# Kernel tuning notes

Hardware: AMD Instinct MI355X
Metric: run time of the kernel (lower is better)

## Reference

```python
import jax, jax.numpy as jnp
import numpy as np

EMBED_DIM = 512


def setup_inputs() -> dict:
    key = jax.random.key(0)
    k1, k2, k3 = jax.random.split(key, 3)
    B, T, E = 8, 2048, EMBED_DIM
    x = jax.random.normal(k1, (B, T, E), dtype=jnp.float32)
    # Linear weights stored [in, out] (torch stores [out, in]; math is identical via transpose)
    Wq = jax.random.normal(k2, (E, E), dtype=jnp.float32) * (E ** -0.5)
    bq = jnp.zeros((E,), dtype=jnp.float32)
    Wk = jax.random.normal(k3, (E, E), dtype=jnp.float32) * (E ** -0.5)
    bk = jnp.zeros((E,), dtype=jnp.float32)
    return {"x": x, "Wq": Wq, "bq": bq, "Wk": Wk, "bk": bk}


def reference(x, Wq, bq, Wk, bk) -> jnp.ndarray:
    scaling = jnp.float32(EMBED_DIM ** -0.5)
    q = (x @ Wq + bq) * scaling          # [B, T, E]
    k = x @ Wk + bk                       # [B, T, E]
    scores = jnp.einsum("bqe,bke->bqk", q, k)   # [B, T, T]
    attn = jax.nn.softmax(scores, axis=-1)
    return jnp.einsum("bqk,bke->bqe", attn, x)  # V = x
```

## Files before the change

kernel.cpp:

```cpp
#include <hip/hip_runtime.h>
#include <hip/hip_bf16.h>
#include <stdint.h>

#define B_  8
#define T_  2048
#define E_  512

typedef __attribute__((ext_vector_type(8))) __bf16 bf16x8;
typedef __attribute__((ext_vector_type(8))) unsigned short ushort8;
typedef __attribute__((ext_vector_type(4))) unsigned short ushort4v;
typedef __attribute__((ext_vector_type(4))) float f32x4;

__device__ __forceinline__ float bf2f(unsigned short u) {
  union { unsigned int u; float f; } c; c.u = ((unsigned int)u) << 16; return c.f;
}
__device__ __forceinline__ unsigned short f2bf(float f) {
  union { float f; unsigned int u; } c; c.f = f;
  unsigned int u = c.u;
  unsigned int r = (u + 0x7FFFu + ((u >> 16) & 1u)) >> 16;
  return (unsigned short)r;
}

__device__ __forceinline__ void gload_lds16(const void* g, void* l) {
  __builtin_amdgcn_global_load_lds(
      (const __attribute__((address_space(1))) uint32_t*)g,
      (__attribute__((address_space(3))) uint32_t*)l, 16, 0, 0);
}

__global__ __launch_bounds__(256)
void trans_conv_kernel(const float* __restrict__ x, unsigned short* __restrict__ xbf,
                       unsigned short* __restrict__ xT) {
  __shared__ unsigned short tile[64][66];
  const int t0 = blockIdx.x * 64, e0 = blockIdx.y * 64, b = blockIdx.z;
  const int tid = threadIdx.x;
  const float* xb = x + ((size_t)b * T_ + t0) * E_ + e0;
  unsigned short* xbf_b = xbf + ((size_t)b * T_ + t0) * E_ + e0;
#pragma unroll
  for (int it = 0; it < 4; ++it) {
    int tr = (tid >> 4) + it * 16;
    int ec = (tid & 15) * 4;
    float4 f = *reinterpret_cast<const float4*>(xb + (size_t)tr * E_ + ec);
    ushort4v o;
    o[0] = f2bf(f.x); o[1] = f2bf(f.y); o[2] = f2bf(f.z); o[3] = f2bf(f.w);
    *reinterpret_cast<ushort4v*>(xbf_b + (size_t)tr * E_ + ec) = o;
    tile[ec + 0][tr] = o[0];
    tile[ec + 1][tr] = o[1];
    tile[ec + 2][tr] = o[2];
    tile[ec + 3][tr] = o[3];
  }
  __syncthreads();
  unsigned short* dst = xT + ((size_t)b * E_ + e0) * T_ + t0;
#pragma unroll
  for (int it = 0; it < 2; ++it) {
    int er = (tid >> 3) + it * 32;
    int tg = (tid & 7) * 8;
    ushort8 r;
#pragma unroll
    for (int j = 0; j < 8; ++j) r[j] = tile[er][tg + j];
    *reinterpret_cast<ushort8*>(dst + (size_t)er * T_ + tg) = r;
  }
}

__global__ __launch_bounds__(256)
void conv_w_kernel(const float* __restrict__ Wq, const float* __restrict__ Wk,
                   const float* __restrict__ bq, const float* __restrict__ bk,
                   unsigned short* __restrict__ WT, float* __restrict__ bqk, float scale) {
  int idx = blockIdx.x * 256 + threadIdx.x;
  int n  = idx >> 9;
  int kk = idx & 511;
  float v = (n < E_) ? Wq[kk * E_ + n] * scale : Wk[kk * E_ + (n - E_)];
  WT[idx] = f2bf(v);
  if (idx < 2 * E_) {
    float bv = (idx < E_) ? bq[idx] * scale : bk[idx - E_];
    bqk[idx] = bv;
  }
}

#define STAGE_A(pbuf, kt) do {                                                  \
  _Pragma("unroll") for (int r_ = 0; r_ < 4; ++r_)                              \
    gload_lds16(gA + (long long)(r_ * 32) * lda + (long long)(kt) * 64,         \
                &sm[(pbuf) * 16384 + r_ * 2048 + tid * 8]);                     \
} while (0)

#define STAGE_B(pbuf, kt) do {                                                  \
  _Pragma("unroll") for (int r_ = 0; r_ < 4; ++r_)                              \
    gload_lds16(gB + (long long)(r_ * 32) * ldb + (long long)(kt) * 64,         \
                &sm[(pbuf) * 16384 + 8192 + r_ * 2048 + tid * 8]);              \
} while (0)

template<int OUT>
__global__ __launch_bounds__(256)
void gemm128c(const unsigned short* __restrict__ A, int lda, long long strA,
              const unsigned short* __restrict__ B, int ldb, long long strB,
              void* __restrict__ Cv, int ldc, long long strC,
              int K, const float* __restrict__ bias, int NBX, int NBY,
              float* __restrict__ Rg, const float* __restrict__ invR)
{
  __shared__ unsigned short sm[32768];
  const int tid  = threadIdx.x;
  const int lane = tid & 63;
  const int wv   = tid >> 6;
  const int wrp  = wv >> 1;
  const int wcp  = wv & 1;
  const int fr   = lane & 15;

  const int nwg = gridDim.x, bid = blockIdx.x;
  const int qq = nwg >> 3, rr = nwg & 7, xc = bid & 7, ii = bid >> 3;
  const int wg = (xc < rr ? xc * (qq + 1) : rr * (qq + 1) + (xc - rr) * qq) + ii;
  const int bx = wg % NBX;
  const int tt = wg / NBX;
  const int by = tt % NBY;
  const int bz = tt / NBY;

  const long long m0 = (long long)by * 128;
  const long long n0 = (long long)bx * 128;
  const unsigned short* Ab = A + (long long)bz * strA + m0 * lda;
  const unsigned short* Bb = B + (long long)bz * strB + n0 * ldb;

  const int srow = tid >> 3;
  const int scol = ((tid & 7) * 8) ^ ((srow & 7) << 3);
  const unsigned short* gA = Ab + (long long)srow * lda + scol;
  const unsigned short* gB = Bb + (long long)srow * ldb + scol;

  const int xorc  = (fr & 7) << 3;
  const int q8    = (lane >> 4) * 8;
  const int c0    = q8 ^ xorc;
  const int c1    = (32 + q8) ^ xorc;
  const int aRow  = (wrp * 64 + fr) * 64;
  const int bRow  = 8192 + (wcp * 64 + fr) * 64;

  f32x4 acc[4][4];
#pragma unroll
  for (int i = 0; i < 4; ++i)
#pragma unroll
    for (int j = 0; j < 4; ++j) acc[i][j] = (f32x4){0.f, 0.f, 0.f, 0.f};

  bf16x8 aA[4][2], bB2[2][2];
  const int NT = K >> 6;

  STAGE_A(0, 0);
  STAGE_B(0, 0);
  STAGE_A(1, 1);
  asm volatile("s_waitcnt vmcnt(4)" ::: "memory");
  __builtin_amdgcn_s_barrier();

  int p = 0;
  for (int t = 0; t < NT; ++t) {
    const int pb = p * 16384;
    const int pn = p ^ 1;
    if (t + 1 < NT) STAGE_B(pn, t + 1);
#pragma unroll
    for (int m = 0; m < 4; ++m) {
      aA[m][0] = *reinterpret_cast<const bf16x8*>(&sm[pb + aRow + m * 1024 + c0]);
      aA[m][1] = *reinterpret_cast<const bf16x8*>(&sm[pb + aRow + m * 1024 + c1]);
    }
#pragma unroll
    for (int n = 0; n < 2; ++n) {
      bB2[n][0] = *reinterpret_cast<const bf16x8*>(&sm[pb + bRow + n * 1024 + c0]);
      bB2[n][1] = *reinterpret_cast<const bf16x8*>(&sm[pb + bRow + n * 1024 + c1]);
    }
    __builtin_amdgcn_s_setprio(1);
#pragma unroll
    for (int m = 0; m < 4; ++m)
#pragma unroll
      for (int n = 0; n < 2; ++n) {
        acc[m][n] = __builtin_amdgcn_mfma_f32_16x16x32_bf16(aA[m][0], bB2[n][0], acc[m][n], 0, 0, 0);
        acc[m][n] = __builtin_amdgcn_mfma_f32_16x16x32_bf16(aA[m][1], bB2[n][1], acc[m][n], 0, 0, 0);
      }
    __builtin_amdgcn_s_setprio(0);
    __builtin_amdgcn_s_barrier();
    if (t + 2 < NT) STAGE_A(p, t + 2);
#pragma unroll
    for (int n = 0; n < 2; ++n) {
      bB2[n][0] = *reinterpret_cast<const bf16x8*>(&sm[pb + bRow + (2 + n) * 1024 + c0]);
      bB2[n][1] = *reinterpret_cast<const bf16x8*>(&sm[pb + bRow + (2 + n) * 1024 + c1]);
    }
    __builtin_amdgcn_s_setprio(1);
#pragma unroll
    for (int m = 0; m < 4; ++m)
#pragma unroll
      for (int n = 0; n < 2; ++n) {
        acc[m][2 + n] = __builtin_amdgcn_mfma_f32_16x16x32_bf16(aA[m][0], bB2[n][0], acc[m][2 + n], 0, 0, 0);
        acc[m][2 + n] = __builtin_amdgcn_mfma_f32_16x16x32_bf16(aA[m][1], bB2[n][1], acc[m][2 + n], 0, 0, 0);
      }
    __builtin_amdgcn_s_setprio(0);
    if (t + 2 < NT) asm volatile("s_waitcnt vmcnt(4)" ::: "memory");
    else            asm volatile("s_waitcnt vmcnt(0)" ::: "memory");
    __builtin_amdgcn_s_barrier();
    p = pn;
  }

  const int rq = (lane >> 4) * 4;
  if (OUT == 2) {
    float* Cb = (float*)Cv + (long long)bz * strC;
#pragma unroll
    for (int m = 0; m < 4; ++m)
#pragma unroll
      for (int j = 0; j < 4; ++j) {
        const int lrow = wrp * 64 + m * 16 + rq + j;
        const long long row = m0 + lrow;
        const float inv = invR[bz * 2048 + row];
#pragma unroll
        for (int n = 0; n < 4; ++n)
          Cb[row * ldc + n0 + wcp * 64 + n * 16 + fr] = acc[m][n][j] * inv;
      }
    return;
  }
  if (OUT == 1) {
#pragma unroll
    for (int m = 0; m < 4; ++m)
#pragma unroll
      for (int n = 0; n < 4; ++n)
#pragma unroll
        for (int j = 0; j < 4; ++j) acc[m][n][j] = __expf(acc[m][n][j]);
    float* rps = (float*)(sm + 17664);
#pragma unroll
    for (int m = 0; m < 4; ++m)
#pragma unroll
      for (int j = 0; j < 4; ++j) {
        float s = acc[m][0][j] + acc[m][1][j] + acc[m][2][j] + acc[m][3][j];
        s += __shfl_xor(s, 1); s += __shfl_xor(s, 2);
        s += __shfl_xor(s, 4); s += __shfl_xor(s, 8);
        if (fr == 0) rps[wcp * 128 + wrp * 64 + m * 16 + rq + j] = s;
      }
  } else if (bias) {
#pragma unroll
    for (int n = 0; n < 4; ++n) {
      const float bv = bias[n0 + wcp * 64 + n * 16 + fr];
#pragma unroll
      for (int m = 0; m < 4; ++m)
#pragma unroll
        for (int j = 0; j < 4; ++j) acc[m][n][j] += bv;
    }
  }
#pragma unroll
  for (int m = 0; m < 4; ++m)
#pragma unroll
    for (int j = 0; j < 4; ++j) {
      const int lrow = wrp * 64 + m * 16 + rq + j;
#pragma unroll
      for (int n = 0; n < 4; ++n)
        sm[lrow * 136 + wcp * 64 + n * 16 + fr] = f2bf(acc[m][n][j]);
    }
  __syncthreads();
  if (OUT == 1) {
    float* rps = (float*)(sm + 17664);
    if (tid < 128) {
      const float s = rps[tid] + rps[128 + tid];
      Rg[((long long)bz * NBX + bx) * 2048 + m0 + tid] = s;
    }
  }
  unsigned short* C = (unsigned short*)Cv + (long long)bz * strC;
#pragma unroll
  for (int it = 0; it < 8; ++it) {
    const int row = it * 16 + (tid >> 4);
    const int chunk = tid & 15;
    ushort8 v = *reinterpret_cast<const ushort8*>(&sm[row * 136 + chunk * 8]);
    *reinterpret_cast<ushort8*>(&C[(m0 + row) * ldc + n0 + chunk * 8]) = v;
  }
}

__global__ __launch_bounds__(256)
void rowsum_inv_kernel(const float* __restrict__ R, float* __restrict__ invR) {
  const int i = blockIdx.x * 256 + threadIdx.x;
  const int b = i >> 11, t = i & 2047;
  float s = 0.f;
#pragma unroll
  for (int c = 0; c < 16; ++c) s += R[((long long)(b * 16 + c)) * 2048 + t];
  invR[i] = 1.0f / s;
}

extern "C" void kernel_launch(void* const* d_in, const int* in_sizes, int n_in,
                              void* d_out, int out_size, void* d_ws, size_t ws_size,
                              hipStream_t stream)
{
  const float* x  = (const float*)d_in[0];
  const float* Wq = (const float*)d_in[1];
  const float* bq = (const float*)d_in[2];
  const float* Wk = (const float*)d_in[3];
  const float* bk = (const float*)d_in[4];
  float* out = (float*)d_out;

  char* w = (char*)d_ws;
  unsigned short* xbf  = (unsigned short*)w;  w += (size_t)B_ * T_ * E_ * 2;
  unsigned short* xT   = (unsigned short*)w;  w += (size_t)B_ * T_ * E_ * 2;
  unsigned short* WT   = (unsigned short*)w;  w += (size_t)2 * E_ * E_ * 2;
  float*          bqk  = (float*)w;           w += (size_t)2 * E_ * 4;
  float*          R    = (float*)w;           w += (size_t)B_ * 16 * T_ * 4;
  float*          invR = (float*)w;           w += (size_t)B_ * T_ * 4;
  unsigned short* qk   = (unsigned short*)w;  w += (size_t)B_ * T_ * 2 * E_ * 2;
  unsigned short* attn = (unsigned short*)w;  w += (size_t)B_ * T_ * T_ * 2;

  const float scale = 0.044194173824159216f;

  trans_conv_kernel<<<dim3(32, 8, 8), 256, 0, stream>>>(x, xbf, xT);
  conv_w_kernel<<<2048, 256, 0, stream>>>(Wq, Wk, bq, bk, WT, bqk, scale);

  gemm128c<0><<<1024, 256, 0, stream>>>(
      xbf, E_, 0, WT, E_, 0, qk, 2 * E_, 0, E_, bqk, 8, 128, nullptr, nullptr);

  gemm128c<1><<<2048, 256, 0, stream>>>(
      qk, 2 * E_, (long long)T_ * 2 * E_,
      qk + E_, 2 * E_, (long long)T_ * 2 * E_,
      attn, T_, (long long)T_ * T_, E_, nullptr, 16, 16, R, nullptr);

  rowsum_inv_kernel<<<64, 256, 0, stream>>>(R, invR);

  gemm128c<2><<<512, 256, 0, stream>>>(
      attn, T_, (long long)T_ * T_,
      xT, T_, (long long)E_ * T_,
      out, E_, (long long)T_ * E_, T_, nullptr, 4, 16, nullptr, invR);
}
```

Baseline: 142.9 us.

## Use 256x128 tiles with 8-wave phased pipeline for projection and score GEMMs

```diff
diff --git a/kernel.cpp b/kernel.cpp
--- a/kernel.cpp
+++ b/kernel.cpp
@@ -76,6 +76,184 @@
   }
 }
 
+#define STG2(gbase, ld, hoff, pbuf, kt) do {                                    \
+  gload_lds16((gbase) + (long long)(kt) * 64,                                   \
+              &sm[(pbuf) * 24576 + (hoff) + wv * 512]);                         \
+  gload_lds16((gbase) + (long long)64 * (ld) + (long long)(kt) * 64,            \
+              &sm[(pbuf) * 24576 + (hoff) + 4096 + wv * 512]);                  \
+} while (0)
+
+#define RD_A4(pp, mh) do {                                                      \
+  const int ab = (pp) * 24576 + (wr * 64 + (mh) * 32 + fr) * 64;                \
+  _Pragma("unroll") for (int m_ = 0; m_ < 2; ++m_) {                            \
+    aA[m_][0] = *reinterpret_cast<const bf16x8*>(&sm[ab + m_ * 1024 + c0]);     \
+    aA[m_][1] = *reinterpret_cast<const bf16x8*>(&sm[ab + m_ * 1024 + c1]);     \
+  } } while (0)
+
+#define RD_B4(pp, nh) do {                                                      \
+  const int bb = (pp) * 24576 + 16384 + (wc * 64 + (nh) * 32 + fr) * 64;        \
+  _Pragma("unroll") for (int n_ = 0; n_ < 2; ++n_) {                            \
+    bB[nh][n_][0] = *reinterpret_cast<const bf16x8*>(&sm[bb + n_ * 1024 + c0]); \
+    bB[nh][n_][1] = *reinterpret_cast<const bf16x8*>(&sm[bb + n_ * 1024 + c1]); \
+  } } while (0)
+
+#define MFMA_Q4(mh, nh) do {                                                    \
+  _Pragma("unroll") for (int m_ = 0; m_ < 2; ++m_)                              \
+  _Pragma("unroll") for (int n_ = 0; n_ < 2; ++n_) {                            \
+    acc[(mh)*2+m_][(nh)*2+n_] = __builtin_amdgcn_mfma_f32_16x16x32_bf16(        \
+        aA[m_][0], bB[nh][n_][0], acc[(mh)*2+m_][(nh)*2+n_], 0, 0, 0);          \
+    acc[(mh)*2+m_][(nh)*2+n_] = __builtin_amdgcn_mfma_f32_16x16x32_bf16(        \
+        aA[m_][1], bB[nh][n_][1], acc[(mh)*2+m_][(nh)*2+n_], 0, 0, 0);          \
+  } } while (0)
+
+template<int DO_EXP>
+__global__ __launch_bounds__(512)
+void gemm4p(const unsigned short* __restrict__ A, int lda, long long strA,
+            const unsigned short* __restrict__ B, int ldb, long long strB,
+            unsigned short* __restrict__ Cg, int ldc, long long strC,
+            int K, const float* __restrict__ bias, int NBX, int NBY,
+            float* __restrict__ Rg)
+{
+  __shared__ unsigned short sm[49152];
+  const int tid  = threadIdx.x;
+  const int lane = tid & 63;
+  const int wv   = tid >> 6;
+  const int wr   = wv >> 1;
+  const int wc   = wv & 1;
+  const int fr   = lane & 15;
+
+  const int nwg = gridDim.x, bid = blockIdx.x;
+  const int qq = nwg >> 3, rr = nwg & 7, xc = bid & 7, ii = bid >> 3;
+  const int wg = (xc < rr ? xc * (qq + 1) : rr * (qq + 1) + (xc - rr) * qq) + ii;
+  const int bx = wg % NBX;
+  const int tt = wg / NBX;
+  const int by = tt % NBY;
+  const int bz = tt / NBY;
+
+  const long long m0 = (long long)by * 256;
+  const long long n0 = (long long)bx * 128;
+  const unsigned short* Ab = A + (long long)bz * strA + m0 * lda;
+  const unsigned short* Bb = B + (long long)bz * strB + n0 * ldb;
+
+  const int srow = tid >> 3;
+  const int scol = ((tid & 7) * 8) ^ ((srow & 7) << 3);
+  const unsigned short* gA0 = Ab + (long long)srow * lda + scol;
+  const unsigned short* gA1 = Ab + (long long)(128 + srow) * lda + scol;
+  const unsigned short* gB  = Bb + (long long)srow * ldb + scol;
+
+  const int xorc = (fr & 7) << 3;
+  const int q8   = (lane >> 4) * 8;
+  const int c0   = q8 ^ xorc;
+  const int c1   = (32 + q8) ^ xorc;
+
+  f32x4 acc[4][4];
+#pragma unroll
+  for (int i = 0; i < 4; ++i)
+#pragma unroll
+    for (int j = 0; j < 4; ++j) acc[i][j] = (f32x4){0.f, 0.f, 0.f, 0.f};
+
+  bf16x8 aA[2][2], bB[2][2][2];
+  const int NT = K >> 6;
+
+  STG2(gA0, lda, 0,     0, 0);
+  STG2(gA1, lda, 8192,  0, 0);
+  STG2(gB,  ldb, 16384, 0, 0);
+  STG2(gB,  ldb, 16384, 1, 1);
+  asm volatile("s_waitcnt vmcnt(2)" ::: "memory");
+  __builtin_amdgcn_s_barrier();
+
+  int p = 0;
+  for (int t = 0; t < NT; ++t) {
+    const int pn = p ^ 1;
+    RD_A4(p, 0);
+    RD_B4(p, 0);
+    if (t + 1 < NT) STG2(gA0, lda, 0, pn, t + 1);
+    __builtin_amdgcn_s_barrier();
+    __builtin_amdgcn_s_setprio(1); MFMA_Q4(0, 0); __builtin_amdgcn_s_setprio(0);
+    __builtin_amdgcn_s_barrier();
+    RD_B4(p, 1);
+    if (t + 1 < NT) STG2(gA1, lda, 8192, pn, t + 1);
+    __builtin_amdgcn_s_barrier();
+    __builtin_amdgcn_s_setprio(1); MFMA_Q4(0, 1); __builtin_amdgcn_s_setprio(0);
+    __builtin_amdgcn_s_barrier();
+    RD_A4(p, 1);
+    if (t + 2 < NT) STG2(gB, ldb, 16384, p, t + 2);
+    __builtin_amdgcn_s_barrier();
+    __builtin_amdgcn_s_setprio(1); MFMA_Q4(1, 0); __builtin_amdgcn_s_setprio(0);
+    __builtin_amdgcn_s_barrier();
+    __builtin_amdgcn_s_setprio(1); MFMA_Q4(1, 1); __builtin_amdgcn_s_setprio(0);
+    if (t + 2 < NT) asm volatile("s_waitcnt vmcnt(2)" ::: "memory");
+    else            asm volatile("s_waitcnt vmcnt(0)" ::: "memory");
+    __builtin_amdgcn_s_barrier();
+    p = pn;
+  }
+
+  const int rq = (lane >> 4) * 4;
+  if (DO_EXP) {
+#pragma unroll
+    for (int m = 0; m < 4; ++m)
+#pragma unroll
+      for (int n = 0; n < 4; ++n)
+#pragma unroll
+        for (int j = 0; j < 4; ++j) acc[m][n][j] = __expf(acc[m][n][j]);
+  } else if (bias) {
+#pragma unroll
+    for (int n = 0; n < 4; ++n) {
+      const float bv = bias[n0 + wc * 64 + n * 16 + fr];
+#pragma unroll
+      for (int m = 0; m < 4; ++m)
+#pragma unroll
+        for (int j = 0; j < 4; ++j) acc[m][n][j] += bv;
+    }
+  }
+  float* rps = (float*)sm;
+  unsigned short* cs = sm + 4096;
+  if (DO_EXP) {
+#pragma unroll
+    for (int m = 0; m < 4; ++m)
+#pragma unroll
+      for (int j = 0; j < 4; ++j) {
+        float s = acc[m][0][j] + acc[m][1][j] + acc[m][2][j] + acc[m][3][j];
+        s += __shfl_xor(s, 1); s += __shfl_xor(s, 2);
+        s += __shfl_xor(s, 4); s += __shfl_xor(s, 8);
+        const int lrow = wr * 64 + m * 16 + rq + j;
+        if (fr == 0) rps[wc * 256 + lrow] = s;
+      }
+  }
+#pragma unroll
+  for (int m = 0; m < 4; ++m)
+#pragma unroll
+    for (int j = 0; j < 4; ++j) {
+      const int lrow = wr * 64 + m * 16 + rq + j;
+#pragma unroll
+      for (int n = 0; n < 4; ++n)
+        cs[lrow * 136 + wc * 64 + n * 16 + fr] = f2bf(acc[m][n][j]);
+    }
+  __syncthreads();
+  if (DO_EXP && tid < 256) {
+    const float s = rps[tid] + rps[256 + tid];
+    Rg[((long long)bz * NBX + bx) * 2048 + m0 + tid] = s;
+  }
+  unsigned short* C = Cg + (long long)bz * strC;
+#pragma unroll
+  for (int it = 0; it < 8; ++it) {
+    const int row = it * 32 + (tid >> 4);
+    const int ch = tid & 15;
+    ushort8 v = *reinterpret_cast<const ushort8*>(&cs[row * 136 + ch * 8]);
+    *reinterpret_cast<ushort8*>(&C[(m0 + row) * ldc + n0 + ch * 8]) = v;
+  }
+}
+
+__global__ __launch_bounds__(256)
+void rowsum_inv_kernel(const float* __restrict__ R, float* __restrict__ invR) {
+  const int i = blockIdx.x * 256 + threadIdx.x;
+  const int b = i >> 11, t = i & 2047;
+  float s = 0.f;
+#pragma unroll
+  for (int c = 0; c < 16; ++c) s += R[((long long)(b * 16 + c)) * 2048 + t];
+  invR[i] = 1.0f / s;
+}
+
 #define STAGE_A(pbuf, kt) do {                                                  \
   _Pragma("unroll") for (int r_ = 0; r_ < 4; ++r_)                              \
     gload_lds16(gA + (long long)(r_ * 32) * lda + (long long)(kt) * 64,         \
@@ -88,13 +266,11 @@
                 &sm[(pbuf) * 16384 + 8192 + r_ * 2048 + tid * 8]);              \
 } while (0)
 
-template<int OUT>
 __global__ __launch_bounds__(256)
-void gemm128c(const unsigned short* __restrict__ A, int lda, long long strA,
-              const unsigned short* __restrict__ B, int ldb, long long strB,
-              void* __restrict__ Cv, int ldc, long long strC,
-              int K, const float* __restrict__ bias, int NBX, int NBY,
-              float* __restrict__ Rg, const float* __restrict__ invR)
+void gemm_pv(const unsigned short* __restrict__ A, int lda, long long strA,
+             const unsigned short* __restrict__ B, int ldb, long long strB,
+             const float* __restrict__ invR,
+             float* __restrict__ C, int ldc, long long strC, int K)
 {
   __shared__ unsigned short sm[32768];
   const int tid  = threadIdx.x;
@@ -107,10 +283,9 @@
   const int nwg = gridDim.x, bid = blockIdx.x;
   const int qq = nwg >> 3, rr = nwg & 7, xc = bid & 7, ii = bid >> 3;
   const int wg = (xc < rr ? xc * (qq + 1) : rr * (qq + 1) + (xc - rr) * qq) + ii;
-  const int bx = wg % NBX;
-  const int tt = wg / NBX;
-  const int by = tt % NBY;
-  const int bz = tt / NBY;
+  const int bx = wg & 3;
+  const int by = (wg >> 2) & 15;
+  const int bz = wg >> 6;
 
   const long long m0 = (long long)by * 128;
   const long long n0 = (long long)bx * 128;
@@ -191,83 +366,18 @@
   }
 
   const int rq = (lane >> 4) * 4;
-  if (OUT == 2) {
-    float* Cb = (float*)Cv + (long long)bz * strC;
-#pragma unroll
-    for (int m = 0; m < 4; ++m)
-#pragma unroll
-      for (int j = 0; j < 4; ++j) {
-        const int lrow = wrp * 64 + m * 16 + rq + j;
-        const long long row = m0 + lrow;
-        const float inv = invR[bz * 2048 + row];
-#pragma unroll
-        for (int n = 0; n < 4; ++n)
-          Cb[row * ldc + n0 + wcp * 64 + n * 16 + fr] = acc[m][n][j] * inv;
-      }
-    return;
-  }
-  if (OUT == 1) {
-#pragma unroll
-    for (int m = 0; m < 4; ++m)
-#pragma unroll
-      for (int n = 0; n < 4; ++n)
-#pragma unroll
-        for (int j = 0; j < 4; ++j) acc[m][n][j] = __expf(acc[m][n][j]);
-    float* rps = (float*)(sm + 17664);
-#pragma unroll
-    for (int m = 0; m < 4; ++m)
-#pragma unroll
-      for (int j = 0; j < 4; ++j) {
-        float s = acc[m][0][j] + acc[m][1][j] + acc[m][2][j] + acc[m][3][j];
-        s += __shfl_xor(s, 1); s += __shfl_xor(s, 2);
-        s += __shfl_xor(s, 4); s += __shfl_xor(s, 8);
-        if (fr == 0) rps[wcp * 128 + wrp * 64 + m * 16 + rq + j] = s;
-      }
-  } else if (bias) {
-#pragma unroll
-    for (int n = 0; n < 4; ++n) {
-      const float bv = bias[n0 + wcp * 64 + n * 16 + fr];
-#pragma unroll
-      for (int m = 0; m < 4; ++m)
-#pragma unroll
-        for (int j = 0; j < 4; ++j) acc[m][n][j] += bv;
-    }
-  }
+  float* Cb = C + (long long)bz * strC;
 #pragma unroll
   for (int m = 0; m < 4; ++m)
 #pragma unroll
     for (int j = 0; j < 4; ++j) {
       const int lrow = wrp * 64 + m * 16 + rq + j;
+      const long long row = m0 + lrow;
+      const float inv = invR[bz * 2048 + row];
 #pragma unroll
       for (int n = 0; n < 4; ++n)
-        sm[lrow * 136 + wcp * 64 + n * 16 + fr] = f2bf(acc[m][n][j]);
-    }
-  __syncthreads();
-  if (OUT == 1) {
-    float* rps = (float*)(sm + 17664);
-    if (tid < 128) {
-      const float s = rps[tid] + rps[128 + tid];
-      Rg[((long long)bz * NBX + bx) * 2048 + m0 + tid] = s;
-    }
-  }
-  unsigned short* C = (unsigned short*)Cv + (long long)bz * strC;
-#pragma unroll
-  for (int it = 0; it < 8; ++it) {
-    const int row = it * 16 + (tid >> 4);
-    const int chunk = tid & 15;
-    ushort8 v = *reinterpret_cast<const ushort8*>(&sm[row * 136 + chunk * 8]);
-    *reinterpret_cast<ushort8*>(&C[(m0 + row) * ldc + n0 + chunk * 8]) = v;
-  }
-}
-
-__global__ __launch_bounds__(256)
-void rowsum_inv_kernel(const float* __restrict__ R, float* __restrict__ invR) {
-  const int i = blockIdx.x * 256 + threadIdx.x;
-  const int b = i >> 11, t = i & 2047;
-  float s = 0.f;
-#pragma unroll
-  for (int c = 0; c < 16; ++c) s += R[((long long)(b * 16 + c)) * 2048 + t];
-  invR[i] = 1.0f / s;
+        Cb[row * ldc + n0 + wcp * 64 + n * 16 + fr] = acc[m][n][j] * inv;
+    }
 }
 
 extern "C" void kernel_launch(void* const* d_in, const int* in_sizes, int n_in,
@@ -296,18 +406,18 @@
   trans_conv_kernel<<<dim3(32, 8, 8), 256, 0, stream>>>(x, xbf, xT);
   conv_w_kernel<<<2048, 256, 0, stream>>>(Wq, Wk, bq, bk, WT, bqk, scale);
 
-  gemm128c<0><<<1024, 256, 0, stream>>>(
-      xbf, E_, 0, WT, E_, 0, qk, 2 * E_, 0, E_, bqk, 8, 128, nullptr, nullptr);
-
-  gemm128c<1><<<2048, 256, 0, stream>>>(
+  gemm4p<0><<<512, 512, 0, stream>>>(
+      xbf, E_, 0, WT, E_, 0, qk, 2 * E_, 0, E_, bqk, 8, 64, nullptr);
+
+  gemm4p<1><<<1024, 512, 0, stream>>>(
       qk, 2 * E_, (long long)T_ * 2 * E_,
       qk + E_, 2 * E_, (long long)T_ * 2 * E_,
-      attn, T_, (long long)T_ * T_, E_, nullptr, 16, 16, R, nullptr);
+      attn, T_, (long long)T_ * T_, E_, nullptr, 16, 8, R);
 
   rowsum_inv_kernel<<<64, 256, 0, stream>>>(R, invR);
 
-  gemm128c<2><<<512, 256, 0, stream>>>(
+  gemm_pv<<<512, 256, 0, stream>>>(
       attn, T_, (long long)T_ * T_,
       xT, T_, (long long)E_ * T_,
-      out, E_, (long long)T_ * E_, T_, nullptr, 4, 16, nullptr, invR);
-}
+      invR, out, E_, (long long)T_ * E_, T_);
+}
```

Measured after the change: 145.9 us. 1.02x slower.

## Restructure GEMM pipeline with triple-buffered A and single barrier per k-step

Applied to the files above, without the earlier changes.

```diff
diff --git a/kernel.cpp b/kernel.cpp
--- a/kernel.cpp
+++ b/kernel.cpp
@@ -76,27 +76,27 @@
   }
 }
 
-#define STAGE_A(pbuf, kt) do {                                                  \
+#define STG_A1(abuf_, kt) do {                                                  \
   _Pragma("unroll") for (int r_ = 0; r_ < 4; ++r_)                              \
     gload_lds16(gA + (long long)(r_ * 32) * lda + (long long)(kt) * 64,         \
-                &sm[(pbuf) * 16384 + r_ * 2048 + tid * 8]);                     \
+                &sm[(abuf_) * 8192 + r_ * 2048 + tid * 8]);                     \
 } while (0)
 
-#define STAGE_B(pbuf, kt) do {                                                  \
+#define STG_B1(bbuf_, kt) do {                                                  \
   _Pragma("unroll") for (int r_ = 0; r_ < 4; ++r_)                              \
     gload_lds16(gB + (long long)(r_ * 32) * ldb + (long long)(kt) * 64,         \
-                &sm[(pbuf) * 16384 + 8192 + r_ * 2048 + tid * 8]);              \
+                &sm[24576 + (bbuf_) * 8192 + r_ * 2048 + tid * 8]);             \
 } while (0)
 
 template<int OUT>
 __global__ __launch_bounds__(256)
-void gemm128c(const unsigned short* __restrict__ A, int lda, long long strA,
-              const unsigned short* __restrict__ B, int ldb, long long strB,
-              void* __restrict__ Cv, int ldc, long long strC,
-              int K, const float* __restrict__ bias, int NBX, int NBY,
-              float* __restrict__ Rg, const float* __restrict__ invR)
+void gemm1b(const unsigned short* __restrict__ A, int lda, long long strA,
+            const unsigned short* __restrict__ B, int ldb, long long strB,
+            void* __restrict__ Cv, int ldc, long long strC,
+            int K, const float* __restrict__ bias, int NBX, int NBY,
+            float* __restrict__ Rg, const float* __restrict__ invR)
 {
-  __shared__ unsigned short sm[32768];
+  __shared__ unsigned short sm[40960];
   const int tid  = threadIdx.x;
   const int lane = tid & 63;
   const int wv   = tid >> 6;
@@ -127,7 +127,7 @@
   const int c0    = q8 ^ xorc;
   const int c1    = (32 + q8) ^ xorc;
   const int aRow  = (wrp * 64 + fr) * 64;
-  const int bRow  = 8192 + (wcp * 64 + fr) * 64;
+  const int bRow  = (wcp * 64 + fr) * 64;
 
   f32x4 acc[4][4];
 #pragma unroll
@@ -135,59 +135,46 @@
 #pragma unroll
     for (int j = 0; j < 4; ++j) acc[i][j] = (f32x4){0.f, 0.f, 0.f, 0.f};
 
-  bf16x8 aA[4][2], bB2[2][2];
+  bf16x8 aA[4][2], bB4[4][2];
   const int NT = K >> 6;
 
-  STAGE_A(0, 0);
-  STAGE_B(0, 0);
-  STAGE_A(1, 1);
+  STG_A1(0, 0);
+  STG_B1(0, 0);
+  STG_A1(1, 1);
   asm volatile("s_waitcnt vmcnt(4)" ::: "memory");
   __builtin_amdgcn_s_barrier();
 
-  int p = 0;
+  int ab = 0;
+  int bb = 0;
   for (int t = 0; t < NT; ++t) {
-    const int pb = p * 16384;
-    const int pn = p ^ 1;
-    if (t + 1 < NT) STAGE_B(pn, t + 1);
+    if (t + 1 < NT) STG_B1(bb ^ 1, t + 1);
+    if (t + 2 < NT) { int ab2 = ab + 2; if (ab2 >= 3) ab2 -= 3; STG_A1(ab2, t + 2); }
+    const int pbA = ab * 8192;
+    const int pbB = 24576 + bb * 8192;
 #pragma unroll
     for (int m = 0; m < 4; ++m) {
-      aA[m][0] = *reinterpret_cast<const bf16x8*>(&sm[pb + aRow + m * 1024 + c0]);
-      aA[m][1] = *reinterpret_cast<const bf16x8*>(&sm[pb + aRow + m * 1024 + c1]);
-    }
-#pragma unroll
-    for (int n = 0; n < 2; ++n) {
-      bB2[n][0] = *reinterpret_cast<const bf16x8*>(&sm[pb + bRow + n * 1024 + c0]);
-      bB2[n][1] = *reinterpret_cast<const bf16x8*>(&sm[pb + bRow + n * 1024 + c1]);
+      aA[m][0] = *reinterpret_cast<const bf16x8*>(&sm[pbA + aRow + m * 1024 + c0]);
+      aA[m][1] = *reinterpret_cast<const bf16x8*>(&sm[pbA + aRow + m * 1024 + c1]);
+    }
+#pragma unroll
+    for (int n = 0; n < 4; ++n) {
+      bB4[n][0] = *reinterpret_cast<const bf16x8*>(&sm[pbB + bRow + n * 1024 + c0]);
+      bB4[n][1] = *reinterpret_cast<const bf16x8*>(&sm[pbB + bRow + n * 1024 + c1]);
     }
     __builtin_amdgcn_s_setprio(1);
 #pragma unroll
     for (int m = 0; m < 4; ++m)
 #pragma unroll
-      for (int n = 0; n < 2; ++n) {
-        acc[m][n] = __builtin_amdgcn_mfma_f32_16x16x32_bf16(aA[m][0], bB2[n][0], acc[m][n], 0, 0, 0);
-        acc[m][n] = __builtin_amdgcn_mfma_f32_16x16x32_bf16(aA[m][1], bB2[n][1], acc[m][n], 0, 0, 0);
+      for (int n = 0; n < 4; ++n) {
+        acc[m][n] = __builtin_amdgcn_mfma_f32_16x16x32_bf16(aA[m][0], bB4[n][0], acc[m][n], 0, 0, 0);
+        acc[m][n] = __builtin_amdgcn_mfma_f32_16x16x32_bf16(aA[m][1], bB4[n][1], acc[m][n], 0, 0, 0);
       }
     __builtin_amdgcn_s_setprio(0);
+    if (t + 2 < NT)      asm volatile("s_waitcnt vmcnt(4)" ::: "memory");
+    else                 asm volatile("s_waitcnt vmcnt(0)" ::: "memory");
     __builtin_amdgcn_s_barrier();
-    if (t + 2 < NT) STAGE_A(p, t + 2);
-#pragma unroll
-    for (int n = 0; n < 2; ++n) {
-      bB2[n][0] = *reinterpret_cast<const bf16x8*>(&sm[pb + bRow + (2 + n) * 1024 + c0]);
-      bB2[n][1] = *reinterpret_cast<const bf16x8*>(&sm[pb + bRow + (2 + n) * 1024 + c1]);
-    }
-    __builtin_amdgcn_s_setprio(1);
-#pragma unroll
-    for (int m = 0; m < 4; ++m)
-#pragma unroll
-      for (int n = 0; n < 2; ++n) {
-        acc[m][2 + n] = __builtin_amdgcn_mfma_f32_16x16x32_bf16(aA[m][0], bB2[n][0], acc[m][2 + n], 0, 0, 0);
-        acc[m][2 + n] = __builtin_amdgcn_mfma_f32_16x16x32_bf16(aA[m][1], bB2[n][1], acc[m][2 + n], 0, 0, 0);
-      }
-    __builtin_amdgcn_s_setprio(0);
-    if (t + 2 < NT) asm volatile("s_waitcnt vmcnt(4)" ::: "memory");
-    else            asm volatile("s_waitcnt vmcnt(0)" ::: "memory");
-    __builtin_amdgcn_s_barrier();
-    p = pn;
+    ab = (ab == 2) ? 0 : ab + 1;
+    bb ^= 1;
   }
 
   const int rq = (lane >> 4) * 4;
@@ -296,17 +283,17 @@
   trans_conv_kernel<<<dim3(32, 8, 8), 256, 0, stream>>>(x, xbf, xT);
   conv_w_kernel<<<2048, 256, 0, stream>>>(Wq, Wk, bq, bk, WT, bqk, scale);
 
-  gemm128c<0><<<1024, 256, 0, stream>>>(
+  gemm1b<0><<<1024, 256, 0, stream>>>(
       xbf, E_, 0, WT, E_, 0, qk, 2 * E_, 0, E_, bqk, 8, 128, nullptr, nullptr);
 
-  gemm128c<1><<<2048, 256, 0, stream>>>(
+  gemm1b<1><<<2048, 256, 0, stream>>>(
       qk, 2 * E_, (long long)T_ * 2 * E_,
       qk + E_, 2 * E_, (long long)T_ * 2 * E_,
       attn, T_, (long long)T_ * T_, E_, nullptr, 16, 16, R, nullptr);
 
   rowsum_inv_kernel<<<64, 256, 0, stream>>>(R, invR);
 
-  gemm128c<2><<<512, 256, 0, stream>>>(
+  gemm1b<2><<<512, 256, 0, stream>>>(
       attn, T_, (long long)T_ * T_,
       xT, T_, (long long)E_ * T_,
       out, E_, (long long)T_ * E_, T_, nullptr, 4, 16, nullptr, invR);
```

Result: no change. 142.5 us (-0.3%).
